# Kernel tuning notes

Measured on AMD Instinct MI355X. Metric: run time of the kernel, lower is better.

The kernel has to match this reference:

```python
import jax, jax.numpy as jnp
import numpy as np

DIM = 2048
NUM_HEADS = 16
HEAD_DIM = 128


def setup_inputs() -> dict:
    key = jax.random.key(0)
    ks = jax.random.split(key, 9)
    B, S = 2, 2048
    s = lambda fan_in: 1.0 / np.sqrt(fan_in)
    return {
        "x": jax.random.normal(ks[0], (B, S, DIM), dtype=jnp.float32),
        "Wq": jax.random.uniform(ks[1], (DIM, NUM_HEADS * HEAD_DIM), jnp.float32, -s(DIM), s(DIM)),
        "bq": jax.random.uniform(ks[2], (NUM_HEADS * HEAD_DIM,), jnp.float32, -s(DIM), s(DIM)),
        "Wk": jax.random.uniform(ks[3], (DIM, HEAD_DIM), jnp.float32, -s(DIM), s(DIM)),
        "bk": jax.random.uniform(ks[4], (HEAD_DIM,), jnp.float32, -s(DIM), s(DIM)),
        "Wv": jax.random.uniform(ks[5], (DIM, HEAD_DIM), jnp.float32, -s(DIM), s(DIM)),
        "bv": jax.random.uniform(ks[6], (HEAD_DIM,), jnp.float32, -s(DIM), s(DIM)),
        "Wo": jax.random.uniform(ks[7], (NUM_HEADS * HEAD_DIM, DIM), jnp.float32, -s(NUM_HEADS * HEAD_DIM), s(NUM_HEADS * HEAD_DIM)),
        "bo": jax.random.uniform(ks[8], (DIM,), jnp.float32, -s(NUM_HEADS * HEAD_DIM), s(NUM_HEADS * HEAD_DIM)),
    }


def reference(x, Wq, bq, Wk, bk, Wv, bv, Wo, bo):
    B, S, _ = x.shape
    H, D = NUM_HEADS, HEAD_DIM
    q = (x @ Wq + bq).reshape(B, S, H, D)          # bnhd
    k = x @ Wk + bk                                 # bmd (single shared KV head)
    v = x @ Wv + bv                                 # bmd
    scale = 1.0 / np.sqrt(D).astype(np.float32)
    scores = jnp.einsum('bnhd,bmd->bnhm', q, k) * scale  # [B,S,H,S]
    attn = jax.nn.softmax(scores, axis=-1)
    out = jnp.einsum('bnhm,bmd->bnhd', attn, v)
    out = out.reshape(B, S, H * D)
    return out @ Wo + bo
```

## Files before the change

### kernel.cpp

```cpp
#include <hip/hip_runtime.h>
#include <cstdint>


#define SEQ 2048
#define NQKV 2304
#define MTOT 4096
#define C2SCALE 0.12752299126446508f

typedef __attribute__((ext_vector_type(8))) short bf16x8;
typedef __attribute__((ext_vector_type(4))) float f32x4;
typedef __attribute__((ext_vector_type(16))) float f32x16;

__device__ __forceinline__ unsigned short cvt_bf16(float f) {
  union { float f; unsigned int u; } v; v.f = f;
  unsigned int r = v.u + 0x7FFFu + ((v.u >> 16) & 1u);
  return (unsigned short)(r >> 16);
}

__device__ __forceinline__ unsigned cvt_pk_bf16(float lo, float hi_) {
  unsigned r;
  asm("v_cvt_pk_bf16_f32 %0, %1, %2" : "=v"(r) : "v"(lo), "v"(hi_));
  return r;
}

__device__ __forceinline__ void plane_swap(unsigned &a, unsigned &b) {
  asm volatile("v_permlane32_swap_b32 %0, %1" : "+v"(a), "+v"(b));
}

__device__ __forceinline__ float exp2_(float x) {
#if __has_builtin(__builtin_amdgcn_exp2f)
  return __builtin_amdgcn_exp2f(x);
#else
  return exp2f(x);
#endif
}

typedef const __attribute__((address_space(1))) void gvoid;
typedef __attribute__((address_space(3))) void lvoid;
__device__ __forceinline__ void gload16(const void* g, void* l) {
  __builtin_amdgcn_global_load_lds((gvoid*)g, (lvoid*)l, 16, 0, 0);
}


__global__ __launch_bounds__(256) void cast_x_kernel(const float* __restrict__ x,
                                                     unsigned short* __restrict__ o) {
  long long i = ((long long)blockIdx.x * 256 + threadIdx.x) * 8;
  float4 a = *(const float4*)(x + i);
  float4 b = *(const float4*)(x + i + 4);
  union { bf16x8 v; unsigned short u[8]; } r;
  r.u[0] = cvt_bf16(a.x); r.u[1] = cvt_bf16(a.y); r.u[2] = cvt_bf16(a.z); r.u[3] = cvt_bf16(a.w);
  r.u[4] = cvt_bf16(b.x); r.u[5] = cvt_bf16(b.y); r.u[6] = cvt_bf16(b.z); r.u[7] = cvt_bf16(b.w);
  *(bf16x8*)(o + i) = r.v;
}

__global__ __launch_bounds__(256) void transpose_cast(
    const float* __restrict__ s0, const float* __restrict__ s1, const float* __restrict__ s2,
    int n1, int n2, int st0, int st1, int st2,
    float sc0, float sc1, float sc2,
    unsigned short* __restrict__ dst, int K) {
  __shared__ float t[32][33];
  int n0 = blockIdx.x * 32, k0 = blockIdx.y * 32;
  const float* src; int off, stride; float sc;
  if (n0 < n1)      { src = s0; off = 0;  stride = st0; sc = sc0; }
  else if (n0 < n2) { src = s1; off = n1; stride = st1; sc = sc1; }
  else              { src = s2; off = n2; stride = st2; sc = sc2; }
  int tx = threadIdx.x & 31, ty = threadIdx.x >> 5;
  #pragma unroll
  for (int r = 0; r < 4; r++)
    t[ty + r * 8][tx] = src[(size_t)(k0 + ty + r * 8) * stride + (n0 - off) + tx] * sc;
  __syncthreads();
  #pragma unroll
  for (int r = 0; r < 4; r++)
    dst[(size_t)(n0 + ty + r * 8) * K + k0 + tx] = cvt_bf16(t[tx][ty + r * 8]);
}

__global__ __launch_bounds__(256) void concat_bias(const float* __restrict__ bq,
    const float* __restrict__ bk, const float* __restrict__ bv, float* __restrict__ b1) {
  int i = blockIdx.x * 256 + threadIdx.x;
  if (i < NQKV)
    b1[i] = (i < 2048) ? bq[i] * C2SCALE : (i < 2176 ? bk[i - 2048] : bv[i - 2176]);
}

__global__ __launch_bounds__(256) void kfrag_prep(const unsigned short* __restrict__ qkv,
                                                  unsigned short* __restrict__ kfrag) {
  int gid = blockIdx.x * 4 + (threadIdx.x >> 6);
  int l = threadIdx.x & 63;
  int b = gid >> 9, rem = gid & 511;
  int jt = rem >> 3, kt = rem & 7;
  const unsigned short* src = qkv + (size_t)(b * 2048 + jt * 32 + (l & 31)) * NQKV
                              + 2048 + kt * 16 + (l >> 5) * 8;
  *(bf16x8*)(kfrag + (size_t)gid * 512 + l * 8) = *(const bf16x8*)src;
}

__global__ __launch_bounds__(256) void vfrag_prep(const unsigned short* __restrict__ qkv,
                                                  unsigned short* __restrict__ vfrag) {
  int gid = blockIdx.x * 4 + (threadIdx.x >> 6);
  int l = threadIdx.x & 63;
  int b = gid >> 9, rem = gid & 511;
  int jt = rem >> 3, s = (rem >> 2) & 1, d0 = rem & 3;
  union { bf16x8 v; unsigned short u[8]; } o;
  #pragma unroll
  for (int e = 0; e < 8; e++)
    o.u[e] = qkv[(size_t)(b * 2048 + jt * 32 + s * 16 + (l >> 5) * 8 + e) * NQKV
                 + 2176 + d0 * 32 + (l & 31)];
  *(bf16x8*)(vfrag + (size_t)gid * 512 + l * 8) = o.v;
}

template <int BF16_OUT>
__global__ __launch_bounds__(256) void gemm_bt(const unsigned short* __restrict__ A,
    const unsigned short* __restrict__ BT, const float* __restrict__ bias,
    void* __restrict__ Cout, int N) {
  __shared__ unsigned short As[128 * 32];
  __shared__ unsigned short Bs[128 * 32];
  const int tid = threadIdx.x;
  const int l = tid & 63, w = tid >> 6;
  const int l15 = l & 15, g = l >> 4;
  const int wr = w >> 1, wc = w & 1;
  const int brow = blockIdx.x * 128, bcol = blockIdx.y * 128;
  const int K = 2048;
  const unsigned short* ga = A + (size_t)(brow + w * 32 + (l >> 2)) * K + (l & 3) * 8;
  const unsigned short* gb = BT + (size_t)(bcol + w * 32 + (l >> 2)) * K + (l & 3) * 8;
  unsigned short* lA = &As[w * 1024];
  unsigned short* lB = &Bs[w * 1024];
  f32x4 acc[4][4];
  const f32x4 z = {0.f, 0.f, 0.f, 0.f};
  #pragma unroll
  for (int i = 0; i < 4; i++)
    #pragma unroll
    for (int j = 0; j < 4; j++) acc[i][j] = z;

  for (int kt = 0; kt < K; kt += 32) {
    gload16(ga + kt, lA);
    gload16(ga + kt + 16 * K, lA + 512);
    gload16(gb + kt, lB);
    gload16(gb + kt + 16 * K, lB + 512);
    __syncthreads();
    bf16x8 af[4], bfr[4];
    #pragma unroll
    for (int mi = 0; mi < 4; mi++)
      af[mi] = *(const bf16x8*)&As[(wr * 64 + mi * 16 + l15) * 32 + g * 8];
    #pragma unroll
    for (int ni = 0; ni < 4; ni++)
      bfr[ni] = *(const bf16x8*)&Bs[(wc * 64 + ni * 16 + l15) * 32 + g * 8];
    __syncthreads();
    #pragma unroll
    for (int mi = 0; mi < 4; mi++)
      #pragma unroll
      for (int ni = 0; ni < 4; ni++)
        acc[mi][ni] = __builtin_amdgcn_mfma_f32_16x16x32_bf16(af[mi], bfr[ni], acc[mi][ni], 0, 0, 0);
  }
  float* Cf = (float*)Cout;
  unsigned short* Cb = (unsigned short*)Cout;
  #pragma unroll
  for (int ni = 0; ni < 4; ni++) {
    int col = bcol + wc * 64 + ni * 16 + l15;
    float bv = bias[col];
    #pragma unroll
    for (int mi = 0; mi < 4; mi++) {
      int row = brow + wr * 64 + mi * 16 + g * 4;
      #pragma unroll
      for (int r = 0; r < 4; r++) {
        float v = acc[mi][ni][r] + bv;
        if (BF16_OUT) Cb[(size_t)(row + r) * N + col] = cvt_bf16(v);
        else          Cf[(size_t)(row + r) * N + col] = v;
      }
    }
  }
}

__global__ __launch_bounds__(64, 1) void attn_kernel(
    const unsigned short* __restrict__ qkv, const unsigned short* __restrict__ kfrag,
    const unsigned short* __restrict__ vfrag, unsigned short* __restrict__ aout) {
  const int l = threadIdx.x, l31 = l & 31, hi = l >> 5;
  const int bid = blockIdx.x;
  const int qt = bid & 31, h = (bid >> 5) & 15, b = bid >> 9;

  bf16x8 qf[2][8];
  #pragma unroll
  for (int q2 = 0; q2 < 2; q2++) {
    const unsigned short* qp =
        qkv + (size_t)(b * 2048 + qt * 64 + q2 * 32 + l31) * NQKV + h * 128 + hi * 8;
    #pragma unroll
    for (int kt = 0; kt < 8; kt++) qf[q2][kt] = *(const bf16x8*)(qp + kt * 16);
  }
  const unsigned short* kp = kfrag + (size_t)b * 262144 + l * 8;
  const unsigned short* vp = vfrag + (size_t)b * 262144 + l * 8;

  f32x16 acc[2][4];
  #pragma unroll
  for (int q2 = 0; q2 < 2; q2++)
    #pragma unroll
    for (int d0 = 0; d0 < 4; d0++)
      #pragma unroll
      for (int r = 0; r < 16; r++) acc[q2][d0][r] = 0.f;
  float lsum[2] = {0.f, 0.f};

  f32x16 zro;
  #pragma unroll
  for (int r = 0; r < 16; r++) zro[r] = 0.f;

  bf16x8 ka[8], kb2[8], va8[8], vb8[8];
  bf16x8 pa_v[2][2];
  f32x16 se0, so0, se1, so1;

#define LOADK(DST, T_) { _Pragma("unroll")                                     \
    for (int u = 0; u < 8; u++)                                                \
      DST[u] = *(const bf16x8*)(kp + (size_t)(T_) * 4096 + u * 512); }
#define LOADV(DST, T_) { _Pragma("unroll")                                     \
    for (int u = 0; u < 8; u++)                                                \
      DST[u] = *(const bf16x8*)(vp + (size_t)(T_) * 4096 + u * 512); }

#define QK2(KC) {                                                              \
    se0 = __builtin_amdgcn_mfma_f32_32x32x16_bf16(KC[0], qf[0][0], zro, 0, 0, 0); \
    so0 = __builtin_amdgcn_mfma_f32_32x32x16_bf16(KC[1], qf[0][1], zro, 0, 0, 0); \
    se1 = __builtin_amdgcn_mfma_f32_32x32x16_bf16(KC[0], qf[1][0], zro, 0, 0, 0); \
    so1 = __builtin_amdgcn_mfma_f32_32x32x16_bf16(KC[1], qf[1][1], zro, 0, 0, 0); \
    _Pragma("unroll")                                                          \
    for (int kt = 1; kt < 4; kt++) {                                           \
      se0 = __builtin_amdgcn_mfma_f32_32x32x16_bf16(KC[2 * kt], qf[0][2 * kt], se0, 0, 0, 0); \
      so0 = __builtin_amdgcn_mfma_f32_32x32x16_bf16(KC[2 * kt + 1], qf[0][2 * kt + 1], so0, 0, 0, 0); \
      se1 = __builtin_amdgcn_mfma_f32_32x32x16_bf16(KC[2 * kt], qf[1][2 * kt], se1, 0, 0, 0); \
      so1 = __builtin_amdgcn_mfma_f32_32x32x16_bf16(KC[2 * kt + 1], qf[1][2 * kt + 1], so1, 0, 0, 0); \
    } }

#define PV2(VB) { _Pragma("unroll")                                            \
    for (int s = 0; s < 2; s++) {                                              \
      _Pragma("unroll")                                                        \
      for (int d0 = 0; d0 < 4; d0++) {                                         \
        acc[0][d0] = __builtin_amdgcn_mfma_f32_32x32x16_bf16(pa_v[0][s], VB[s * 4 + d0], acc[0][d0], 0, 0, 0); \
        acc[1][d0] = __builtin_amdgcn_mfma_f32_32x32x16_bf16(pa_v[1][s], VB[s * 4 + d0], acc[1][d0], 0, 0, 0); \
      } } }

#define SM1(SE, SO, Q2) {                                                      \
    float p_[16];                                                              \
    _Pragma("unroll")                                                          \
    for (int r = 0; r < 16; r++) p_[r] = exp2_(SE[r] + SO[r]);                 \
    float s01_ = p_[0] + p_[1],   s23_ = p_[2] + p_[3];                        \
    float s45_ = p_[4] + p_[5],   s67_ = p_[6] + p_[7];                        \
    float s89_ = p_[8] + p_[9],   sab_ = p_[10] + p_[11];                      \
    float scd_ = p_[12] + p_[13], sef_ = p_[14] + p_[15];                      \
    float q0_ = s01_ + s23_, q1_ = s45_ + s67_;                                \
    float q2_ = s89_ + sab_, q3_ = scd_ + sef_;                                \
    float rs_ = (q0_ + q1_) + (q2_ + q3_);                                     \
    rs_ += __shfl_xor(rs_, 32);                                                \
    lsum[Q2] += rs_;                                                           \
    _Pragma("unroll")                                                          \
    for (int s = 0; s < 2; s++) {                                              \
      unsigned a0_ = cvt_pk_bf16(p_[s * 8 + 0], p_[s * 8 + 1]);                \
      unsigned b0_ = cvt_pk_bf16(p_[s * 8 + 4], p_[s * 8 + 5]);                \
      plane_swap(a0_, b0_);                                                    \
      unsigned a1_ = cvt_pk_bf16(p_[s * 8 + 2], p_[s * 8 + 3]);                \
      unsigned b1_ = cvt_pk_bf16(p_[s * 8 + 6], p_[s * 8 + 7]);                \
      plane_swap(a1_, b1_);                                                    \
      union { bf16x8 v; unsigned u[4]; } pa_;                                  \
      pa_.u[0] = a0_; pa_.u[1] = a1_; pa_.u[2] = b0_; pa_.u[3] = b1_;          \
      pa_v[Q2][s] = pa_.v;                                                     \
    } }
#define SM2() { SM1(se0, so0, 0); SM1(se1, so1, 1); }

  LOADK(ka, 0); LOADK(kb2, 1); LOADV(va8, 0); LOADV(vb8, 1);
  QK2(ka); SM2();

  for (int jt2 = 0; jt2 < 31; jt2++) {
    const int t0 = 2 * jt2;
    QK2(kb2); PV2(va8); LOADK(ka, t0 + 2); LOADV(va8, t0 + 2); SM2();
    QK2(ka); PV2(vb8); LOADK(kb2, t0 + 3); LOADV(vb8, t0 + 3); SM2();
  }
  QK2(kb2); PV2(va8); SM2();
  PV2(vb8);

#undef LOADK
#undef LOADV
#undef QK2
#undef PV2
#undef SM1
#undef SM2

  #pragma unroll
  for (int q2 = 0; q2 < 2; q2++) {
    float linv = 1.0f / lsum[q2];
    const int qrow0 = b * 2048 + qt * 64 + q2 * 32;
    #pragma unroll
    for (int r = 0; r < 16; r++) {
      const int crow = (r & 3) + 8 * (r >> 2) + 4 * hi;
      float li = __shfl(linv, crow);
      size_t rbase = (size_t)(qrow0 + crow) * 2048 + h * 128 + l31;
      #pragma unroll
      for (int d0 = 0; d0 < 4; d0++)
        aout[rbase + d0 * 32] = cvt_bf16(acc[q2][d0][r] * li);
    }
  }
}


extern "C" void kernel_launch(void* const* d_in, const int* in_sizes, int n_in,
                              void* d_out, int out_size, void* d_ws, size_t ws_size,
                              hipStream_t stream) {
  const float* x  = (const float*)d_in[0];
  const float* Wq = (const float*)d_in[1];
  const float* bq = (const float*)d_in[2];
  const float* Wk = (const float*)d_in[3];
  const float* bk = (const float*)d_in[4];
  const float* Wv = (const float*)d_in[5];
  const float* bv = (const float*)d_in[6];
  const float* Wo = (const float*)d_in[7];
  const float* bo = (const float*)d_in[8];
  float* out = (float*)d_out;

  char* ws = (char*)d_ws;
  size_t off = 0;
  auto alloc = [&](size_t bytes) -> void* {
    void* p = ws + off;
    off += (bytes + 255) & ~(size_t)255;
    return p;
  };
  unsigned short* xb     = (unsigned short*)alloc((size_t)MTOT * 2048 * 2);
  unsigned short* W1T    = (unsigned short*)alloc((size_t)NQKV * 2048 * 2);
  unsigned short* WoT    = (unsigned short*)alloc((size_t)2048 * 2048 * 2);
  float*          bias1  = (float*)alloc((size_t)NQKV * 4);
  unsigned short* qkv    = (unsigned short*)alloc((size_t)MTOT * NQKV * 2);
  unsigned short* kfragb = (unsigned short*)alloc((size_t)2 * 262144 * 2);
  unsigned short* vfragb = (unsigned short*)alloc((size_t)2 * 262144 * 2);
  unsigned short* aoutb  = (unsigned short*)alloc((size_t)MTOT * 2048 * 2);
  if (off > ws_size) return;

  cast_x_kernel<<<4096, 256, 0, stream>>>(x, xb);
  transpose_cast<<<dim3(72, 64), 256, 0, stream>>>(Wq, Wk, Wv, 2048, 2176,
                                                   2048, 128, 128,
                                                   C2SCALE, 1.0f, 1.0f,
                                                   W1T, 2048);
  transpose_cast<<<dim3(64, 64), 256, 0, stream>>>(Wo, Wo, Wo, 2048, 2048,
                                                   2048, 2048, 2048,
                                                   1.0f, 1.0f, 1.0f,
                                                   WoT, 2048);
  concat_bias<<<9, 256, 0, stream>>>(bq, bk, bv, bias1);

  gemm_bt<1><<<dim3(32, 18), 256, 0, stream>>>(xb, W1T, bias1, qkv, NQKV);
  kfrag_prep<<<256, 256, 0, stream>>>(qkv, kfragb);
  vfrag_prep<<<256, 256, 0, stream>>>(qkv, vfragb);
  attn_kernel<<<1024, 64, 0, stream>>>(qkv, kfragb, vfragb, aoutb);
  gemm_bt<0><<<dim3(32, 16), 256, 0, stream>>>(aoutb, WoT, bo, out, 2048);
}
```

Before: 193.9 us.

## Merge prep kernels into one launch and scatter K/V fragments from QKV GEMM epilogue

Combines the x cast, the weight transposes and the bias concat into a single prep kernel, so the launch count drops from four to one. The QKV GEMM epilogue now writes Q into a compact buffer and scatters K and V directly into the fragment layouts the attention kernel expects. This removes the separate kfrag/vfrag prep kernels and their extra read of the qkv buffer. The scattered 2-byte stores in the epilogue are uncoalesced, which may slow the K/V column blocks of the GEMM.

After: 218.1 us. +12.5%, slower.

```diff
diff --git a/kernel.cpp b/kernel.cpp
--- a/kernel.cpp
+++ b/kernel.cpp
@@ -4,6 +4,7 @@
 
 #define SEQ 2048
 #define NQKV 2304
+#define QD 2048
 #define MTOT 4096
 #define C2SCALE 0.12752299126446508f
 
@@ -41,75 +42,61 @@
   __builtin_amdgcn_global_load_lds((gvoid*)g, (lvoid*)l, 16, 0, 0);
 }
 
-
-__global__ __launch_bounds__(256) void cast_x_kernel(const float* __restrict__ x,
-                                                     unsigned short* __restrict__ o) {
-  long long i = ((long long)blockIdx.x * 256 + threadIdx.x) * 8;
-  float4 a = *(const float4*)(x + i);
-  float4 b = *(const float4*)(x + i + 4);
-  union { bf16x8 v; unsigned short u[8]; } r;
-  r.u[0] = cvt_bf16(a.x); r.u[1] = cvt_bf16(a.y); r.u[2] = cvt_bf16(a.z); r.u[3] = cvt_bf16(a.w);
-  r.u[4] = cvt_bf16(b.x); r.u[5] = cvt_bf16(b.y); r.u[6] = cvt_bf16(b.z); r.u[7] = cvt_bf16(b.w);
-  *(bf16x8*)(o + i) = r.v;
-}
-
-__global__ __launch_bounds__(256) void transpose_cast(
-    const float* __restrict__ s0, const float* __restrict__ s1, const float* __restrict__ s2,
-    int n1, int n2, int st0, int st1, int st2,
-    float sc0, float sc1, float sc2,
-    unsigned short* __restrict__ dst, int K) {
+__global__ __launch_bounds__(256) void prep_kernel(
+    const float* __restrict__ x,
+    const float* __restrict__ Wq, const float* __restrict__ Wk,
+    const float* __restrict__ Wv, const float* __restrict__ Wo,
+    const float* __restrict__ bq, const float* __restrict__ bk,
+    const float* __restrict__ bv,
+    unsigned short* __restrict__ xb, unsigned short* __restrict__ W1T,
+    unsigned short* __restrict__ WoT, float* __restrict__ b1) {
   __shared__ float t[32][33];
-  int n0 = blockIdx.x * 32, k0 = blockIdx.y * 32;
-  const float* src; int off, stride; float sc;
-  if (n0 < n1)      { src = s0; off = 0;  stride = st0; sc = sc0; }
-  else if (n0 < n2) { src = s1; off = n1; stride = st1; sc = sc1; }
-  else              { src = s2; off = n2; stride = st2; sc = sc2; }
-  int tx = threadIdx.x & 31, ty = threadIdx.x >> 5;
-  #pragma unroll
-  for (int r = 0; r < 4; r++)
-    t[ty + r * 8][tx] = src[(size_t)(k0 + ty + r * 8) * stride + (n0 - off) + tx] * sc;
-  __syncthreads();
-  #pragma unroll
-  for (int r = 0; r < 4; r++)
-    dst[(size_t)(n0 + ty + r * 8) * K + k0 + tx] = cvt_bf16(t[tx][ty + r * 8]);
-}
-
-__global__ __launch_bounds__(256) void concat_bias(const float* __restrict__ bq,
-    const float* __restrict__ bk, const float* __restrict__ bv, float* __restrict__ b1) {
-  int i = blockIdx.x * 256 + threadIdx.x;
+  const int bid = blockIdx.x, tid = threadIdx.x;
+  if (bid < 4096) {
+    long long i = ((long long)bid * 256 + tid) * 8;
+    float4 a = *(const float4*)(x + i);
+    float4 b = *(const float4*)(x + i + 4);
+    union { bf16x8 v; unsigned short u[8]; } r;
+    r.u[0] = cvt_bf16(a.x); r.u[1] = cvt_bf16(a.y); r.u[2] = cvt_bf16(a.z); r.u[3] = cvt_bf16(a.w);
+    r.u[4] = cvt_bf16(b.x); r.u[5] = cvt_bf16(b.y); r.u[6] = cvt_bf16(b.z); r.u[7] = cvt_bf16(b.w);
+    *(bf16x8*)(xb + i) = r.v;
+    return;
+  }
+  if (bid < 12800) {
+    int n0, k0, off, stride;
+    const float* src; float sc; unsigned short* dst;
+    if (bid < 8704) {
+      int idx = bid - 4096;
+      n0 = (idx % 72) * 32; k0 = (idx / 72) * 32;
+      if (n0 < 2048)      { src = Wq; off = 0;    stride = 2048; sc = C2SCALE; }
+      else if (n0 < 2176) { src = Wk; off = 2048; stride = 128;  sc = 1.0f; }
+      else                { src = Wv; off = 2176; stride = 128;  sc = 1.0f; }
+      dst = W1T;
+    } else {
+      int idx = bid - 8704;
+      n0 = (idx & 63) * 32; k0 = (idx >> 6) * 32;
+      src = Wo; off = 0; stride = 2048; sc = 1.0f;
+      dst = WoT;
+    }
+    int tx = tid & 31, ty = tid >> 5;
+    #pragma unroll
+    for (int r = 0; r < 4; r++)
+      t[ty + r * 8][tx] = src[(size_t)(k0 + ty + r * 8) * stride + (n0 - off) + tx] * sc;
+    __syncthreads();
+    #pragma unroll
+    for (int r = 0; r < 4; r++)
+      dst[(size_t)(n0 + ty + r * 8) * 2048 + k0 + tx] = cvt_bf16(t[tx][ty + r * 8]);
+    return;
+  }
+  int i = (bid - 12800) * 256 + tid;
   if (i < NQKV)
     b1[i] = (i < 2048) ? bq[i] * C2SCALE : (i < 2176 ? bk[i - 2048] : bv[i - 2176]);
 }
 
-__global__ __launch_bounds__(256) void kfrag_prep(const unsigned short* __restrict__ qkv,
-                                                  unsigned short* __restrict__ kfrag) {
-  int gid = blockIdx.x * 4 + (threadIdx.x >> 6);
-  int l = threadIdx.x & 63;
-  int b = gid >> 9, rem = gid & 511;
-  int jt = rem >> 3, kt = rem & 7;
-  const unsigned short* src = qkv + (size_t)(b * 2048 + jt * 32 + (l & 31)) * NQKV
-                              + 2048 + kt * 16 + (l >> 5) * 8;
-  *(bf16x8*)(kfrag + (size_t)gid * 512 + l * 8) = *(const bf16x8*)src;
-}
-
-__global__ __launch_bounds__(256) void vfrag_prep(const unsigned short* __restrict__ qkv,
-                                                  unsigned short* __restrict__ vfrag) {
-  int gid = blockIdx.x * 4 + (threadIdx.x >> 6);
-  int l = threadIdx.x & 63;
-  int b = gid >> 9, rem = gid & 511;
-  int jt = rem >> 3, s = (rem >> 2) & 1, d0 = rem & 3;
-  union { bf16x8 v; unsigned short u[8]; } o;
-  #pragma unroll
-  for (int e = 0; e < 8; e++)
-    o.u[e] = qkv[(size_t)(b * 2048 + jt * 32 + s * 16 + (l >> 5) * 8 + e) * NQKV
-                 + 2176 + d0 * 32 + (l & 31)];
-  *(bf16x8*)(vfrag + (size_t)gid * 512 + l * 8) = o.v;
-}
-
-template <int BF16_OUT>
-__global__ __launch_bounds__(256) void gemm_bt(const unsigned short* __restrict__ A,
+__global__ __launch_bounds__(256) void gemm_qkv(const unsigned short* __restrict__ A,
     const unsigned short* __restrict__ BT, const float* __restrict__ bias,
-    void* __restrict__ Cout, int N) {
+    unsigned short* __restrict__ qb, unsigned short* __restrict__ kfrag,
+    unsigned short* __restrict__ vfrag) {
   __shared__ unsigned short As[128 * 32];
   __shared__ unsigned short Bs[128 * 32];
   const int tid = threadIdx.x;
@@ -149,8 +136,80 @@
       for (int ni = 0; ni < 4; ni++)
         acc[mi][ni] = __builtin_amdgcn_mfma_f32_16x16x32_bf16(af[mi], bfr[ni], acc[mi][ni], 0, 0, 0);
   }
-  float* Cf = (float*)Cout;
-  unsigned short* Cb = (unsigned short*)Cout;
+  #pragma unroll
+  for (int ni = 0; ni < 4; ni++) {
+    const int col = bcol + wc * 64 + ni * 16 + l15;
+    const float bv = bias[col];
+    #pragma unroll
+    for (int mi = 0; mi < 4; mi++) {
+      const int row0 = brow + wr * 64 + mi * 16 + g * 4;
+      #pragma unroll
+      for (int r = 0; r < 4; r++) {
+        const int row = row0 + r;
+        const unsigned short hv = cvt_bf16(acc[mi][ni][r] + bv);
+        if (bcol < 2048) {
+          qb[(size_t)row * QD + col] = hv;
+        } else if (bcol < 2176) {
+          const int d = col - 2048;
+          const int b = row >> 11, j = row & 2047;
+          const int jt = j >> 5, jl = j & 31;
+          const int kt = d >> 4, hi2 = (d >> 3) & 1, e = d & 7;
+          kfrag[(size_t)(((b * 64 + jt) * 8 + kt)) * 512 + (jl + 32 * hi2) * 8 + e] = hv;
+        } else {
+          const int d = col - 2176;
+          const int b = row >> 11, j = row & 2047;
+          const int jt = j >> 5, jr = j & 31;
+          const int s = jr >> 4, hi2 = (jr >> 3) & 1, e2 = jr & 7;
+          const int d0 = d >> 5, lv = d & 31;
+          vfrag[(size_t)(((b * 64 + jt) * 8 + s * 4 + d0)) * 512 + (lv + 32 * hi2) * 8 + e2] = hv;
+        }
+      }
+    }
+  }
+}
+
+__global__ __launch_bounds__(256) void gemm_out(const unsigned short* __restrict__ A,
+    const unsigned short* __restrict__ BT, const float* __restrict__ bias,
+    float* __restrict__ Cf, int N) {
+  __shared__ unsigned short As[128 * 32];
+  __shared__ unsigned short Bs[128 * 32];
+  const int tid = threadIdx.x;
+  const int l = tid & 63, w = tid >> 6;
+  const int l15 = l & 15, g = l >> 4;
+  const int wr = w >> 1, wc = w & 1;
+  const int brow = blockIdx.x * 128, bcol = blockIdx.y * 128;
+  const int K = 2048;
+  const unsigned short* ga = A + (size_t)(brow + w * 32 + (l >> 2)) * K + (l & 3) * 8;
+  const unsigned short* gb = BT + (size_t)(bcol + w * 32 + (l >> 2)) * K + (l & 3) * 8;
+  unsigned short* lA = &As[w * 1024];
+  unsigned short* lB = &Bs[w * 1024];
+  f32x4 acc[4][4];
+  const f32x4 z = {0.f, 0.f, 0.f, 0.f};
+  #pragma unroll
+  for (int i = 0; i < 4; i++)
+    #pragma unroll
+    for (int j = 0; j < 4; j++) acc[i][j] = z;
+
+  for (int kt = 0; kt < K; kt += 32) {
+    gload16(ga + kt, lA);
+    gload16(ga + kt + 16 * K, lA + 512);
+    gload16(gb + kt, lB);
+    gload16(gb + kt + 16 * K, lB + 512);
+    __syncthreads();
+    bf16x8 af[4], bfr[4];
+    #pragma unroll
+    for (int mi = 0; mi < 4; mi++)
+      af[mi] = *(const bf16x8*)&As[(wr * 64 + mi * 16 + l15) * 32 + g * 8];
+    #pragma unroll
+    for (int ni = 0; ni < 4; ni++)
+      bfr[ni] = *(const bf16x8*)&Bs[(wc * 64 + ni * 16 + l15) * 32 + g * 8];
+    __syncthreads();
+    #pragma unroll
+    for (int mi = 0; mi < 4; mi++)
+      #pragma unroll
+      for (int ni = 0; ni < 4; ni++)
+        acc[mi][ni] = __builtin_amdgcn_mfma_f32_16x16x32_bf16(af[mi], bfr[ni], acc[mi][ni], 0, 0, 0);
+  }
   #pragma unroll
   for (int ni = 0; ni < 4; ni++) {
     int col = bcol + wc * 64 + ni * 16 + l15;
@@ -159,17 +218,14 @@
     for (int mi = 0; mi < 4; mi++) {
       int row = brow + wr * 64 + mi * 16 + g * 4;
       #pragma unroll
-      for (int r = 0; r < 4; r++) {
-        float v = acc[mi][ni][r] + bv;
-        if (BF16_OUT) Cb[(size_t)(row + r) * N + col] = cvt_bf16(v);
-        else          Cf[(size_t)(row + r) * N + col] = v;
-      }
+      for (int r = 0; r < 4; r++)
+        Cf[(size_t)(row + r) * N + col] = acc[mi][ni][r] + bv;
     }
   }
 }
 
 __global__ __launch_bounds__(64, 1) void attn_kernel(
-    const unsigned short* __restrict__ qkv, const unsigned short* __restrict__ kfrag,
+    const unsigned short* __restrict__ qb, const unsigned short* __restrict__ kfrag,
     const unsigned short* __restrict__ vfrag, unsigned short* __restrict__ aout) {
   const int l = threadIdx.x, l31 = l & 31, hi = l >> 5;
   const int bid = blockIdx.x;
@@ -179,7 +235,7 @@
   #pragma unroll
   for (int q2 = 0; q2 < 2; q2++) {
     const unsigned short* qp =
-        qkv + (size_t)(b * 2048 + qt * 64 + q2 * 32 + l31) * NQKV + h * 128 + hi * 8;
+        qb + (size_t)(b * 2048 + qt * 64 + q2 * 32 + l31) * QD + h * 128 + hi * 8;
     #pragma unroll
     for (int kt = 0; kt < 8; kt++) qf[q2][kt] = *(const bf16x8*)(qp + kt * 16);
   }
@@ -318,26 +374,15 @@
   unsigned short* W1T    = (unsigned short*)alloc((size_t)NQKV * 2048 * 2);
   unsigned short* WoT    = (unsigned short*)alloc((size_t)2048 * 2048 * 2);
   float*          bias1  = (float*)alloc((size_t)NQKV * 4);
-  unsigned short* qkv    = (unsigned short*)alloc((size_t)MTOT * NQKV * 2);
+  unsigned short* qbuf   = (unsigned short*)alloc((size_t)MTOT * QD * 2);
   unsigned short* kfragb = (unsigned short*)alloc((size_t)2 * 262144 * 2);
   unsigned short* vfragb = (unsigned short*)alloc((size_t)2 * 262144 * 2);
   unsigned short* aoutb  = (unsigned short*)alloc((size_t)MTOT * 2048 * 2);
   if (off > ws_size) return;
 
-  cast_x_kernel<<<4096, 256, 0, stream>>>(x, xb);
-  transpose_cast<<<dim3(72, 64), 256, 0, stream>>>(Wq, Wk, Wv, 2048, 2176,
-                                                   2048, 128, 128,
-                                                   C2SCALE, 1.0f, 1.0f,
-                                                   W1T, 2048);
-  transpose_cast<<<dim3(64, 64), 256, 0, stream>>>(Wo, Wo, Wo, 2048, 2048,
-                                                   2048, 2048, 2048,
-                                                   1.0f, 1.0f, 1.0f,
-                                                   WoT, 2048);
-  concat_bias<<<9, 256, 0, stream>>>(bq, bk, bv, bias1);
-
-  gemm_bt<1><<<dim3(32, 18), 256, 0, stream>>>(xb, W1T, bias1, qkv, NQKV);
-  kfrag_prep<<<256, 256, 0, stream>>>(qkv, kfragb);
-  vfrag_prep<<<256, 256, 0, stream>>>(qkv, vfragb);
-  attn_kernel<<<1024, 64, 0, stream>>>(qkv, kfragb, vfragb, aoutb);
-  gemm_bt<0><<<dim3(32, 16), 256, 0, stream>>>(aoutb, WoT, bo, out, 2048);
-}
+  prep_kernel<<<12809, 256, 0, stream>>>(x, Wq, Wk, Wv, Wo, bq, bk, bv,
+                                         xb, W1T, WoT, bias1);
+  gemm_qkv<<<dim3(32, 18), 256, 0, stream>>>(xb, W1T, bias1, qbuf, kfragb, vfragb);
+  attn_kernel<<<1024, 64, 0, stream>>>(qbuf, kfragb, vfragb, aoutb);
+  gemm_out<<<dim3(32, 16), 256, 0, stream>>>(aoutb, WoT, bo, out, 2048);
+}
```
